# Kernel optimization log

Hardware: AMD Instinct MI355X
Metric: run time of the kernel (lower is better)

## Reference

```python
import jax, jax.numpy as jnp
import numpy as np
import math

B, T, F, H, A = 32, 2048, 2048, 1024, 512


def setup_inputs() -> dict:
    key = jax.random.key(0)
    ks = jax.random.split(key, 8)
    def xavier(k, shape):
        fan_out, fan_in = shape
        bound = math.sqrt(6.0 / (fan_in + fan_out))
        return jax.random.uniform(k, shape, jnp.float32, -bound, bound)
    return {
        "features": jax.random.normal(ks[0], (B, T, F), jnp.float32),
        "hidden": jax.random.normal(ks[1], (B, H), jnp.float32),
        "W_h": xavier(ks[2], (A, H)),
        "b_h": jnp.zeros((A,), jnp.float32),
        "W_a": xavier(ks[3], (A, F)),
        "b_a": jnp.zeros((A,), jnp.float32),
        "v_w": xavier(ks[4], (1, A)),
        "v_b": jnp.zeros((1,), jnp.float32),
    }


def reference(features, hidden, W_h, b_h, W_a, b_a, v_w, v_b):
    # h_proj: [B, 1, A]; a_proj: [B, T, A]
    h_proj = (hidden @ W_h.T + b_h)[:, None, :]
    a_proj = jnp.einsum('btf,af->bta', features, W_a) + b_a
    # energy: [B, T]
    energy = (jnp.tanh(h_proj + a_proj) @ v_w[0] + v_b[0]) / math.sqrt(W_h.shape[0])
    alpha = jax.nn.softmax(energy, axis=1)
    context = jnp.einsum('bt,btf->bf', alpha, features)
    return (context, alpha)
```

## Files before the change

kernel.cpp:

```cpp
#include <hip/hip_runtime.h>
#include <hip/hip_bf16.h>
#include <math.h>

#define B_ 32
#define T_ 2048
#define F_ 2048
#define H_ 1024
#define A_ 512

typedef __attribute__((ext_vector_type(8))) short short8;
typedef __attribute__((ext_vector_type(4))) float f32x4;

__device__ __forceinline__ unsigned short f2bf(float x) {
  union { float f; unsigned int u; } v; v.f = x;
  unsigned int r = v.u + 0x7FFFu + ((v.u >> 16) & 1u);
  return (unsigned short)(r >> 16);
}

#define GLOAD_LDS16(gp, lp) __builtin_amdgcn_global_load_lds( \
    (const __attribute__((address_space(1))) void*)(gp), \
    (__attribute__((address_space(3))) void*)(lp), 16, 0, 0)

#define SBAR   asm volatile("s_barrier" ::: "memory")
#define SCHEDB __builtin_amdgcn_sched_barrier(0)
#define WAIT_V1_L0 asm volatile("s_waitcnt vmcnt(1) lgkmcnt(0)" ::: "memory")

__global__ __launch_bounds__(256) void k_convert_wa(const float* __restrict__ wa,
                                                    unsigned short* __restrict__ out) {
  int i = (blockIdx.x * 256 + threadIdx.x) * 4;
  float4 v = *(const float4*)(wa + i);
  ushort4 o;
  o.x = f2bf(v.x); o.y = f2bf(v.y); o.z = f2bf(v.z); o.w = f2bf(v.w);
  *(ushort4*)(out + i) = o;
}

__global__ __launch_bounds__(256) void k_hproj(const float* __restrict__ hidden,
                                               const float* __restrict__ Wh,
                                               const float* __restrict__ bh,
                                               const float* __restrict__ ba,
                                               float* __restrict__ hcomb) {
  int gw = (blockIdx.x * 256 + threadIdx.x) >> 6;
  int lane = threadIdx.x & 63;
  int b = gw >> 9, a = gw & 511;
  const float* wr = Wh + a * H_;
  const float* hr = hidden + b * H_;
  float acc = 0.f;
  #pragma unroll
  for (int k = 0; k < H_; k += 256) {
    float4 wv = *(const float4*)(wr + k + lane * 4);
    float4 hv = *(const float4*)(hr + k + lane * 4);
    acc += wv.x * hv.x + wv.y * hv.y + wv.z * hv.z + wv.w * hv.w;
  }
  #pragma unroll
  for (int off = 32; off; off >>= 1) acc += __shfl_xor(acc, off);
  if (lane == 0) hcomb[gw] = acc + bh[a] + ba[a];
}

__global__ __launch_bounds__(512, 4) void k_energy(
    const float* __restrict__ feat, const unsigned short* __restrict__ wab,
    const float* __restrict__ hcomb, const float* __restrict__ vw,
    const float* __restrict__ vb, float* __restrict__ energy) {
  __shared__ __align__(16) char smem[78848];

  const int tid = threadIdx.x;
  const int lane = tid & 63;
  const int w = tid >> 6;
  const int wm = w >> 2, wn = w & 3;
  const int lrow = lane & 15, lk = lane >> 4;
  const int m0 = blockIdx.x * 64;
  const int bb = m0 >> 11;

  float* s_h = (float*)(smem + 73728);
  float* s_v = (float*)(smem + 75776);

  const unsigned short* bsrc0 = wab + (size_t)(tid >> 2) * 2048 +
      ((((tid & 3) - ((tid >> 3) & 3)) & 3) << 3);
  const float* asrc = feat + (size_t)(m0 + (tid >> 3)) * 2048 + ((tid & 7) << 2);
  const int aw_off = ((tid >> 3) << 6) +
      ((((((tid >> 1) & 3) + ((tid >> 4) & 3)) & 3)) << 4) + ((tid & 1) << 3);

  const int psl = ((lk + (lrow >> 1)) & 3) << 4;
  const int a_roff = ((wm * 32 + lrow) << 6) + psl;
  const int b_roff = ((wn * 128 + lrow) << 6) + psl;

  f32x4 acc[2][8] = {};
  float4 avA, avB;

  s_h[tid] = hcomb[bb * 512 + tid];
  s_v[tid] = vw[tid];
  {
    avA = *(const float4*)(asrc);
    char* bd = smem + (w << 10);
    GLOAD_LDS16(bsrc0,              bd);
    GLOAD_LDS16(bsrc0 + 128 * 2048, bd + 8192);
    GLOAD_LDS16(bsrc0 + 256 * 2048, bd + 16384);
    GLOAD_LDS16(bsrc0 + 384 * 2048, bd + 24576);
    SCHEDB;
    avB = *(const float4*)(asrc + 32);
    SCHEDB;
    ushort4 ap;
    ap.x = f2bf(avA.x); ap.y = f2bf(avA.y); ap.z = f2bf(avA.z); ap.w = f2bf(avA.w);
    *(ushort4*)(smem + 65536 + aw_off) = ap;
    SCHEDB;
    WAIT_V1_L0;
    SBAR;
  }

#define ENERGY_BODY(CUR, NXT, CONS, SLOT, K1, K2) do {                        \
    const unsigned short* bs_ = bsrc0 + (K1);                                 \
    char* bd_ = smem + (NXT) * 32768 + (w << 10);                             \
    GLOAD_LDS16(bs_,              bd_);                                       \
    GLOAD_LDS16(bs_ + 128 * 2048, bd_ + 8192);                                \
    GLOAD_LDS16(bs_ + 256 * 2048, bd_ + 16384);                               \
    GLOAD_LDS16(bs_ + 384 * 2048, bd_ + 24576);                               \
    SCHEDB;                                                                   \
    {                                                                         \
      const char* Ab = smem + 65536 + (CUR) * 4096 + a_roff;                  \
      const char* Bb = smem + (CUR) * 32768 + b_roff;                         \
      short8 a0 = *(const short8*)(Ab);                                       \
      short8 a1 = *(const short8*)(Ab + 1024);                                \
      short8 b0 = *(const short8*)(Bb);                                       \
      short8 b1 = *(const short8*)(Bb + 1024);                                \
      short8 b2 = *(const short8*)(Bb + 2048);                                \
      short8 b3 = *(const short8*)(Bb + 3072);                                \
      acc[0][0] = __builtin_amdgcn_mfma_f32_16x16x32_bf16(a0, b0, acc[0][0], 0, 0, 0); \
      acc[1][0] = __builtin_amdgcn_mfma_f32_16x16x32_bf16(a1, b0, acc[1][0], 0, 0, 0); \
      acc[0][1] = __builtin_amdgcn_mfma_f32_16x16x32_bf16(a0, b1, acc[0][1], 0, 0, 0); \
      acc[1][1] = __builtin_amdgcn_mfma_f32_16x16x32_bf16(a1, b1, acc[1][1], 0, 0, 0); \
      acc[0][2] = __builtin_amdgcn_mfma_f32_16x16x32_bf16(a0, b2, acc[0][2], 0, 0, 0); \
      acc[1][2] = __builtin_amdgcn_mfma_f32_16x16x32_bf16(a1, b2, acc[1][2], 0, 0, 0); \
      acc[0][3] = __builtin_amdgcn_mfma_f32_16x16x32_bf16(a0, b3, acc[0][3], 0, 0, 0); \
      acc[1][3] = __builtin_amdgcn_mfma_f32_16x16x32_bf16(a1, b3, acc[1][3], 0, 0, 0); \
      short8 b4 = *(const short8*)(Bb + 4096);                                \
      short8 b5 = *(const short8*)(Bb + 5120);                                \
      short8 b6 = *(const short8*)(Bb + 6144);                                \
      short8 b7 = *(const short8*)(Bb + 7168);                                \
      acc[0][4] = __builtin_amdgcn_mfma_f32_16x16x32_bf16(a0, b4, acc[0][4], 0, 0, 0); \
      acc[1][4] = __builtin_amdgcn_mfma_f32_16x16x32_bf16(a1, b4, acc[1][4], 0, 0, 0); \
      acc[0][5] = __builtin_amdgcn_mfma_f32_16x16x32_bf16(a0, b5, acc[0][5], 0, 0, 0); \
      acc[1][5] = __builtin_amdgcn_mfma_f32_16x16x32_bf16(a1, b5, acc[1][5], 0, 0, 0); \
      acc[0][6] = __builtin_amdgcn_mfma_f32_16x16x32_bf16(a0, b6, acc[0][6], 0, 0, 0); \
      acc[1][6] = __builtin_amdgcn_mfma_f32_16x16x32_bf16(a1, b6, acc[1][6], 0, 0, 0); \
      acc[0][7] = __builtin_amdgcn_mfma_f32_16x16x32_bf16(a0, b7, acc[0][7], 0, 0, 0); \
      acc[1][7] = __builtin_amdgcn_mfma_f32_16x16x32_bf16(a1, b7, acc[1][7], 0, 0, 0); \
    }                                                                         \
    {                                                                         \
      ushort4 ap_;       \
      ap_.x = f2bf((CONS).x); ap_.y = f2bf((CONS).y);                         \
      ap_.z = f2bf((CONS).z); ap_.w = f2bf((CONS).w);                         \
      *(ushort4*)(smem + 65536 + (NXT) * 4096 + aw_off) = ap_;                \
    }                                                                         \
    SCHEDB;                                                                   \
    (SLOT) = *(const float4*)(asrc + (K2));               \
    SCHEDB;                                                                   \
    WAIT_V1_L0;    \
    SBAR;                                                                     \
  } while (0)

  #pragma unroll 1
  for (int t = 0; t < 64; t += 2) {
    ENERGY_BODY(0, 1, avB, avA, (((t + 1) & 63) << 5), (((t + 2) & 63) << 5));
    ENERGY_BODY(1, 0, avA, avB, (((t + 2) & 63) << 5), (((t + 3) & 63) << 5));
  }
#undef ENERGY_BODY

  float (*e_red)[4] = (float(*)[4])(smem + 77824);
  const float vbv = vb[0];
  #pragma unroll
  for (int mi = 0; mi < 2; ++mi) {
    #pragma unroll
    for (int j = 0; j < 4; ++j) {
      float s = 0.f;
      #pragma unroll
      for (int ni = 0; ni < 8; ++ni) {
        int col = wn * 128 + ni * 16 + lrow;
        float x = acc[mi][ni][j] + s_h[col];
        s += tanhf(x) * s_v[col];
      }
      s += __shfl_xor(s, 1); s += __shfl_xor(s, 2);
      s += __shfl_xor(s, 4); s += __shfl_xor(s, 8);
      if (lrow == 0) e_red[wm * 32 + mi * 16 + (lane >> 4) * 4 + j][wn] = s;
    }
  }
  __syncthreads();
  if (tid < 64) {
    float s = e_red[tid][0] + e_red[tid][1] + e_red[tid][2] + e_red[tid][3];
    energy[m0 + tid] = (s + vbv) * 0.04419417382415922f;
  }
}

__global__ __launch_bounds__(256) void k_softmax(const float* __restrict__ energy,
                                                 float* __restrict__ alpha) {
  const int b = blockIdx.x, tid = threadIdx.x;
  const float* e = energy + b * T_;
  float4 v0 = ((const float4*)e)[tid * 2];
  float4 v1 = ((const float4*)e)[tid * 2 + 1];
  float m = fmaxf(fmaxf(fmaxf(v0.x, v0.y), fmaxf(v0.z, v0.w)),
                  fmaxf(fmaxf(v1.x, v1.y), fmaxf(v1.z, v1.w)));
  #pragma unroll
  for (int off = 32; off; off >>= 1) m = fmaxf(m, __shfl_xor(m, off));
  __shared__ float rmax[4], rsum[4];
  const int lane = tid & 63, wv = tid >> 6;
  if (!lane) rmax[wv] = m;
  __syncthreads();
  m = fmaxf(fmaxf(rmax[0], rmax[1]), fmaxf(rmax[2], rmax[3]));
  float x0 = expf(v0.x - m), x1 = expf(v0.y - m), x2 = expf(v0.z - m), x3 = expf(v0.w - m);
  float x4 = expf(v1.x - m), x5 = expf(v1.y - m), x6 = expf(v1.z - m), x7 = expf(v1.w - m);
  float s = ((x0 + x1) + (x2 + x3)) + ((x4 + x5) + (x6 + x7));
  #pragma unroll
  for (int off = 32; off; off >>= 1) s += __shfl_xor(s, off);
  if (!lane) rsum[wv] = s;
  __syncthreads();
  s = (rsum[0] + rsum[1]) + (rsum[2] + rsum[3]);
  float inv = 1.f / s;
  float4 o0 = {x0 * inv, x1 * inv, x2 * inv, x3 * inv};
  float4 o1 = {x4 * inv, x5 * inv, x6 * inv, x7 * inv};
  float* ao = alpha + b * T_;
  ((float4*)ao)[tid * 2] = o0;
  ((float4*)ao)[tid * 2 + 1] = o1;
}

__global__ __launch_bounds__(256) void k_ctx_partial(const float* __restrict__ feat,
                                                     const float* __restrict__ alpha,
                                                     float* __restrict__ part) {
  const int b = blockIdx.x, fh = blockIdx.y, tc = blockIdx.z;
  const int tid = threadIdx.x;
  __shared__ float sa[128];
  if (tid < 128) sa[tid] = alpha[b * T_ + tc * 128 + tid];
  __syncthreads();
  const int f = fh * 1024 + tid * 4;
  const float* fp = feat + ((size_t)(b * T_ + tc * 128)) * F_ + f;
  float4 s = {0.f, 0.f, 0.f, 0.f};
  #pragma unroll 4
  for (int t = 0; t < 128; ++t) {
    float a = sa[t];
    float4 v = *(const float4*)(fp + (size_t)t * F_);
    s.x += a * v.x; s.y += a * v.y; s.z += a * v.z; s.w += a * v.w;
  }
  *(float4*)(part + ((size_t)(b * 16 + tc)) * F_ + f) = s;
}

__global__ __launch_bounds__(256) void k_ctx_reduce(const float* __restrict__ part,
                                                    float* __restrict__ ctx) {
  const int i4 = blockIdx.x * 256 + threadIdx.x;
  const int b = i4 >> 9, f4 = i4 & 511;
  const float4* p = (const float4*)part;
  float4 s = {0.f, 0.f, 0.f, 0.f};
  #pragma unroll
  for (int tc = 0; tc < 16; ++tc) {
    float4 v = p[((b * 16 + tc) << 9) + f4];
    s.x += v.x; s.y += v.y; s.z += v.z; s.w += v.w;
  }
  ((float4*)ctx)[i4] = s;
}

extern "C" void kernel_launch(void* const* d_in, const int* in_sizes, int n_in,
                              void* d_out, int out_size, void* d_ws, size_t ws_size,
                              hipStream_t stream) {
  const float* feat   = (const float*)d_in[0];
  const float* hidden = (const float*)d_in[1];
  const float* Wh     = (const float*)d_in[2];
  const float* bh     = (const float*)d_in[3];
  const float* Wa     = (const float*)d_in[4];
  const float* ba     = (const float*)d_in[5];
  const float* vw     = (const float*)d_in[6];
  const float* vb     = (const float*)d_in[7];

  float* ctx   = (float*)d_out;
  float* alpha = (float*)d_out + B_ * T_;

  char* ws = (char*)d_ws;
  unsigned short* wab = (unsigned short*)ws;
  float* hcomb  = (float*)(ws + 2097152);
  float* energy = (float*)(ws + 2097152 + 65536);
  float* part   = (float*)(ws + 2097152 + 65536 + 262144);

  k_convert_wa<<<dim3(1024), dim3(256), 0, stream>>>(Wa, wab);
  k_hproj<<<dim3(4096), dim3(256), 0, stream>>>(hidden, Wh, bh, ba, hcomb);
  k_energy<<<dim3(1024), dim3(512), 0, stream>>>(feat, wab, hcomb, vw, vb, energy);
  k_softmax<<<dim3(32), dim3(256), 0, stream>>>(energy, alpha);
  k_ctx_partial<<<dim3(32, 2, 16), dim3(256), 0, stream>>>(feat, alpha, part);
  k_ctx_reduce<<<dim3(64), dim3(256), 0, stream>>>(part, ctx);
}
```

Measured before the change: 343.9 us.

## Widen energy GEMM K-tile to 64 with XOR-swizzled LDS and single-buffered weights

Restructures the energy GEMM main loop. Each iteration now covers a K step of 64 instead of 32, so there are half as many barriers. The bf16 weight tile sits in a single 64KB LDS buffer and the feature tile is double-buffered, both using an XOR swizzle to avoid bank conflicts. The h-projection and v vectors are now read into registers for the epilogue instead of staged in LDS. The cost is that weight DMA loads are issued only after a barrier that follows compute and are waited on before the next tile, so the weight transfer no longer overlaps with the MFMA work.

```diff
diff --git a/kernel.cpp b/kernel.cpp
--- a/kernel.cpp
+++ b/kernel.cpp
@@ -23,7 +23,6 @@
 
 #define SBAR   asm volatile("s_barrier" ::: "memory")
 #define SCHEDB __builtin_amdgcn_sched_barrier(0)
-#define WAIT_V1_L0 asm volatile("s_waitcnt vmcnt(1) lgkmcnt(0)" ::: "memory")
 
 __global__ __launch_bounds__(256) void k_convert_wa(const float* __restrict__ wa,
                                                     unsigned short* __restrict__ out) {
@@ -60,69 +59,59 @@
     const float* __restrict__ feat, const unsigned short* __restrict__ wab,
     const float* __restrict__ hcomb, const float* __restrict__ vw,
     const float* __restrict__ vb, float* __restrict__ energy) {
-  __shared__ __align__(16) char smem[78848];
+  __shared__ __align__(16) char smem[81920];
 
   const int tid = threadIdx.x;
   const int lane = tid & 63;
   const int w = tid >> 6;
   const int wm = w >> 2, wn = w & 3;
-  const int lrow = lane & 15, lk = lane >> 4;
+  const int lrow = lane & 15;
   const int m0 = blockIdx.x * 64;
   const int bb = m0 >> 11;
 
-  float* s_h = (float*)(smem + 73728);
-  float* s_v = (float*)(smem + 75776);
-
-  const unsigned short* bsrc0 = wab + (size_t)(tid >> 2) * 2048 +
-      ((((tid & 3) - ((tid >> 3) & 3)) & 3) << 3);
-  const float* asrc = feat + (size_t)(m0 + (tid >> 3)) * 2048 + ((tid & 7) << 2);
-  const int aw_off = ((tid >> 3) << 6) +
-      ((((((tid >> 1) & 3) + ((tid >> 4) & 3)) & 3)) << 4) + ((tid & 1) << 3);
-
-  const int psl = ((lk + (lrow >> 1)) & 3) << 4;
-  const int a_roff = ((wm * 32 + lrow) << 6) + psl;
-  const int b_roff = ((wn * 128 + lrow) << 6) + psl;
+  const int brow = tid >> 3;
+  const unsigned short* const bsrc0 = wab + (size_t)brow * 2048 +
+      (((((tid & 7) << 4) ^ ((brow & 7) << 4)) >> 1));
+  char* const ldsb = smem + w * 1024;
+
+  const int arow = tid >> 3;
+  const float* const asrc = feat + (size_t)(m0 + arow) * F_ + ((tid & 7) << 3);
+  const int aw_byte = (arow << 7) + ((((tid & 7) << 4)) ^ ((arow & 7) << 4));
+
+  const int xbase = ((lane >> 4) << 4) ^ ((lane & 7) << 4);
+  const int a_row_byte = (wm * 32 + lrow) << 7;
+  const int b_row_byte = (wn * 128 + lrow) << 7;
 
   f32x4 acc[2][8] = {};
-  float4 avA, avB;
-
-  s_h[tid] = hcomb[bb * 512 + tid];
-  s_v[tid] = vw[tid];
+
   {
-    avA = *(const float4*)(asrc);
-    char* bd = smem + (w << 10);
-    GLOAD_LDS16(bsrc0,              bd);
-    GLOAD_LDS16(bsrc0 + 128 * 2048, bd + 8192);
-    GLOAD_LDS16(bsrc0 + 256 * 2048, bd + 16384);
-    GLOAD_LDS16(bsrc0 + 384 * 2048, bd + 24576);
-    SCHEDB;
-    avB = *(const float4*)(asrc + 32);
-    SCHEDB;
-    ushort4 ap;
-    ap.x = f2bf(avA.x); ap.y = f2bf(avA.y); ap.z = f2bf(avA.z); ap.w = f2bf(avA.w);
-    *(ushort4*)(smem + 65536 + aw_off) = ap;
-    SCHEDB;
-    WAIT_V1_L0;
-    SBAR;
-  }
-
-#define ENERGY_BODY(CUR, NXT, CONS, SLOT, K1, K2) do {                        \
-    const unsigned short* bs_ = bsrc0 + (K1);                                 \
-    char* bd_ = smem + (NXT) * 32768 + (w << 10);                             \
-    GLOAD_LDS16(bs_,              bd_);                                       \
-    GLOAD_LDS16(bs_ + 128 * 2048, bd_ + 8192);                                \
-    GLOAD_LDS16(bs_ + 256 * 2048, bd_ + 16384);                               \
-    GLOAD_LDS16(bs_ + 384 * 2048, bd_ + 24576);                               \
-    SCHEDB;                                                                   \
-    {                                                                         \
-      const char* Ab = smem + 65536 + (CUR) * 4096 + a_roff;                  \
-      const char* Bb = smem + (CUR) * 32768 + b_roff;                         \
+    float4 av0 = *(const float4*)(asrc);
+    float4 av1 = *(const float4*)(asrc + 4);
+    #pragma unroll
+    for (int r = 0; r < 8; ++r)
+      GLOAD_LDS16(bsrc0 + r * (64 * 2048), ldsb + r * 8192);
+    short8 apk;
+    apk[0] = (short)f2bf(av0.x); apk[1] = (short)f2bf(av0.y);
+    apk[2] = (short)f2bf(av0.z); apk[3] = (short)f2bf(av0.w);
+    apk[4] = (short)f2bf(av1.x); apk[5] = (short)f2bf(av1.y);
+    apk[6] = (short)f2bf(av1.z); apk[7] = (short)f2bf(av1.w);
+    *(short8*)(smem + 65536 + aw_byte) = apk;
+    __syncthreads();
+  }
+
+#define COMPUTE_TILE(CURBUF) do {                                             \
+    const char* As_ = smem + 65536 + (CURBUF) * 8192;                         \
+    _Pragma("unroll")                                                         \
+    for (int kk = 0; kk < 2; ++kk) {                                          \
+      const int xo = xbase ^ (kk << 6);                                       \
+      const char* Ab = As_ + a_row_byte + xo;                                 \
+      const char* Bb = smem + b_row_byte + xo;                                \
       short8 a0 = *(const short8*)(Ab);                                       \
-      short8 a1 = *(const short8*)(Ab + 1024);                                \
+      short8 a1 = *(const short8*)(Ab + 2048);                                \
       short8 b0 = *(const short8*)(Bb);                                       \
-      short8 b1 = *(const short8*)(Bb + 1024);                                \
-      short8 b2 = *(const short8*)(Bb + 2048);                                \
-      short8 b3 = *(const short8*)(Bb + 3072);                                \
+      short8 b1 = *(const short8*)(Bb + 2048);                                \
+      short8 b2 = *(const short8*)(Bb + 4096);                                \
+      short8 b3 = *(const short8*)(Bb + 6144);                                \
       acc[0][0] = __builtin_amdgcn_mfma_f32_16x16x32_bf16(a0, b0, acc[0][0], 0, 0, 0); \
       acc[1][0] = __builtin_amdgcn_mfma_f32_16x16x32_bf16(a1, b0, acc[1][0], 0, 0, 0); \
       acc[0][1] = __builtin_amdgcn_mfma_f32_16x16x32_bf16(a0, b1, acc[0][1], 0, 0, 0); \
@@ -131,10 +120,10 @@
       acc[1][2] = __builtin_amdgcn_mfma_f32_16x16x32_bf16(a1, b2, acc[1][2], 0, 0, 0); \
       acc[0][3] = __builtin_amdgcn_mfma_f32_16x16x32_bf16(a0, b3, acc[0][3], 0, 0, 0); \
       acc[1][3] = __builtin_amdgcn_mfma_f32_16x16x32_bf16(a1, b3, acc[1][3], 0, 0, 0); \
-      short8 b4 = *(const short8*)(Bb + 4096);                                \
-      short8 b5 = *(const short8*)(Bb + 5120);                                \
-      short8 b6 = *(const short8*)(Bb + 6144);                                \
-      short8 b7 = *(const short8*)(Bb + 7168);                                \
+      short8 b4 = *(const short8*)(Bb + 8192);                                \
+      short8 b5 = *(const short8*)(Bb + 10240);                               \
+      short8 b6 = *(const short8*)(Bb + 12288);                               \
+      short8 b7 = *(const short8*)(Bb + 14336);                               \
       acc[0][4] = __builtin_amdgcn_mfma_f32_16x16x32_bf16(a0, b4, acc[0][4], 0, 0, 0); \
       acc[1][4] = __builtin_amdgcn_mfma_f32_16x16x32_bf16(a1, b4, acc[1][4], 0, 0, 0); \
       acc[0][5] = __builtin_amdgcn_mfma_f32_16x16x32_bf16(a0, b5, acc[0][5], 0, 0, 0); \
@@ -144,27 +133,41 @@
       acc[0][7] = __builtin_amdgcn_mfma_f32_16x16x32_bf16(a0, b7, acc[0][7], 0, 0, 0); \
       acc[1][7] = __builtin_amdgcn_mfma_f32_16x16x32_bf16(a1, b7, acc[1][7], 0, 0, 0); \
     }                                                                         \
-    {                                                                         \
-      ushort4 ap_;       \
-      ap_.x = f2bf((CONS).x); ap_.y = f2bf((CONS).y);                         \
-      ap_.z = f2bf((CONS).z); ap_.w = f2bf((CONS).w);                         \
-      *(ushort4*)(smem + 65536 + (NXT) * 4096 + aw_off) = ap_;                \
-    }                                                                         \
-    SCHEDB;                                                                   \
-    (SLOT) = *(const float4*)(asrc + (K2));               \
-    SCHEDB;                                                                   \
-    WAIT_V1_L0;    \
-    SBAR;                                                                     \
   } while (0)
 
   #pragma unroll 1
-  for (int t = 0; t < 64; t += 2) {
-    ENERGY_BODY(0, 1, avB, avA, (((t + 1) & 63) << 5), (((t + 2) & 63) << 5));
-    ENERGY_BODY(1, 0, avA, avB, (((t + 2) & 63) << 5), (((t + 3) & 63) << 5));
-  }
-#undef ENERGY_BODY
-
-  float (*e_red)[4] = (float(*)[4])(smem + 77824);
+  for (int t = 0; t < 31; ++t) {
+    const int cur = t & 1, nxt = cur ^ 1;
+    const int k1 = (t + 1) << 6;
+    float4 av0 = *(const float4*)(asrc + k1);
+    float4 av1 = *(const float4*)(asrc + k1 + 4);
+    SCHEDB;
+    COMPUTE_TILE(cur);
+    SBAR;
+    const unsigned short* bs = bsrc0 + k1;
+    #pragma unroll
+    for (int r = 0; r < 8; ++r)
+      GLOAD_LDS16(bs + r * (64 * 2048), ldsb + r * 8192);
+    short8 apk;
+    apk[0] = (short)f2bf(av0.x); apk[1] = (short)f2bf(av0.y);
+    apk[2] = (short)f2bf(av0.z); apk[3] = (short)f2bf(av0.w);
+    apk[4] = (short)f2bf(av1.x); apk[5] = (short)f2bf(av1.y);
+    apk[6] = (short)f2bf(av1.z); apk[7] = (short)f2bf(av1.w);
+    *(short8*)(smem + 65536 + nxt * 8192 + aw_byte) = apk;
+    __syncthreads();
+  }
+  COMPUTE_TILE(1);
+#undef COMPUTE_TILE
+
+  float hv[8], vv[8];
+  #pragma unroll
+  for (int ni = 0; ni < 8; ++ni) {
+    int col = wn * 128 + ni * 16 + lrow;
+    hv[ni] = hcomb[bb * 512 + col];
+    vv[ni] = vw[col];
+  }
+  float (*e_red)[4] = (float(*)[4])(smem + 65536);
+  __syncthreads();
   const float vbv = vb[0];
   #pragma unroll
   for (int mi = 0; mi < 2; ++mi) {
@@ -173,9 +176,8 @@
       float s = 0.f;
       #pragma unroll
       for (int ni = 0; ni < 8; ++ni) {
-        int col = wn * 128 + ni * 16 + lrow;
-        float x = acc[mi][ni][j] + s_h[col];
-        s += tanhf(x) * s_v[col];
+        float x = acc[mi][ni][j] + hv[ni];
+        s += tanhf(x) * vv[ni];
       }
       s += __shfl_xor(s, 1); s += __shfl_xor(s, 2);
       s += __shfl_xor(s, 4); s += __shfl_xor(s, 8);
```

Result: faster. 299.9 us (-12.8%).
